# Optimization experiments

Hardware: AMD Instinct MI355X
Metric: run time of the kernel (lower is better)

The kernel has to match this reference:

```python
import jax, jax.numpy as jnp
import numpy as np

E = 384      # embed_dim
H = 8        # num_heads
D = E // H   # head_dim = 48
G = 16       # grid_size
HT = 128     # height
WD = 128     # width
FF = 1536
B = 8
EPS = 1e-5


def _ln(x, g, b):
    m = jnp.mean(x, axis=-1, keepdims=True)
    v = jnp.mean(jnp.square(x - m), axis=-1, keepdims=True)
    return (x - m) * jax.lax.rsqrt(v + EPS) * g + b


def _grid_attention(xn, in_proj_w, in_proj_b, out_w, out_b):
    # xn: [B, S, E] with S = HT*WD. Extract 16x16 windows -> [Wn, B, T, E]
    nh, nw = HT // G, WD // G
    T = G * G
    xw = xn.reshape(B, nh, G, nw, G, E).transpose(1, 3, 0, 2, 4, 5)
    xw = xw.reshape(nh * nw, B, T, E)  # [Wn, B, T, E]
    # torch in_proj: qkv = x @ W.T + b, W: [3E, E]
    qkv = jnp.einsum('wbte,fe->wbtf', xw, in_proj_w) + in_proj_b
    q, k, v = jnp.split(qkv, 3, axis=-1)
    q = q.reshape(nh * nw, B, T, H, D)
    k = k.reshape(nh * nw, B, T, H, D)
    v = v.reshape(nh * nw, B, T, H, D)
    scale = 1.0 / jnp.sqrt(jnp.asarray(D, dtype=xn.dtype))
    # NOTE: torch MHA (batch_first=False) treats dim0 of (B, T, E) as seq len,
    # so attention mixes across the batch axis (length B) per window position.
    scores = jnp.einsum('wbtnd,wctnd->wtnbc', q, k) * scale  # [Wn,T,H,B,B]
    p = jax.nn.softmax(scores, axis=-1)
    o = jnp.einsum('wtnbc,wctnd->wbtnd', p, v).reshape(nh * nw, B, T, E)
    o = jnp.einsum('wbte,fe->wbtf', o, out_w) + out_b
    # reassemble windows back to [B, S, E]
    o = o.reshape(nh, nw, B, G, G, E).transpose(2, 0, 3, 1, 4, 5)
    return o.reshape(B, HT * WD, E)


def setup_inputs() -> dict:
    key = jax.random.key(0)
    ks = jax.random.split(key, 6)
    S = HT * WD
    return {
        'x': jax.random.normal(ks[0], (B, S, E), jnp.float32),
        'in_proj_w': jax.random.normal(ks[1], (3 * E, E), jnp.float32) * 0.02,
        'in_proj_b': jnp.zeros((3 * E,), jnp.float32),
        'out_w': jax.random.normal(ks[2], (E, E), jnp.float32) * 0.02,
        'out_b': jnp.zeros((E,), jnp.float32),
        'ln1_g': jnp.ones((E,), jnp.float32),
        'ln1_b': jnp.zeros((E,), jnp.float32),
        'ln2_g': jnp.ones((E,), jnp.float32),
        'ln2_b': jnp.zeros((E,), jnp.float32),
        'w1': jax.random.normal(ks[3], (FF, E), jnp.float32) * 0.02,
        'b1': jnp.zeros((FF,), jnp.float32),
        'w2': jax.random.normal(ks[4], (E, FF), jnp.float32) * 0.02,
        'b2': jnp.zeros((E,), jnp.float32),
    }


def reference(x, in_proj_w, in_proj_b, out_w, out_b, ln1_g, ln1_b,
              ln2_g, ln2_b, w1, b1, w2, b2):
    # Pre-attn LN, windowed MHA (eval mode: dropout off), residual
    attn = _grid_attention(_ln(x, ln1_g, ln1_b), in_proj_w, in_proj_b, out_w, out_b)
    x = x + attn
    # LN + GELU MLP (exact erf gelu, torch nn.GELU default) + residual
    h = _ln(x, ln2_g, ln2_b)
    h = jax.nn.gelu(jnp.einsum('bse,fe->bsf', h, w1) + b1, approximate=False)
    h = jnp.einsum('bsf,ef->bse', h, w2) + b2
    return x + h
```

## Files before the change

kernel.cpp:

```cpp
#include <hip/hip_runtime.h>
#include <hip/hip_bf16.h>
#include <math.h>

typedef unsigned short u16;
typedef __attribute__((ext_vector_type(8))) short short8;
typedef __attribute__((ext_vector_type(4))) float floatx4;

__device__ __forceinline__ float bf2f(u16 u) {
  union { unsigned int i; float f; } w; w.i = ((unsigned int)u) << 16; return w.f;
}
__device__ __forceinline__ u16 f2bf(float f) {
  union { float f; unsigned int i; } w; w.f = f;
  unsigned int r = (w.i + 0x7fffu + ((w.i >> 16) & 1u)) >> 16;
  return (u16)r;
}

__global__ void detect_k(const unsigned int* __restrict__ xw, int* __restrict__ flag) {
  __shared__ int cnt;
  if (threadIdx.x == 0) cnt = 0;
  __syncthreads();
  int c = 0;
  for (int i = threadIdx.x; i < 4096; i += 256) {
    const unsigned int e = (xw[i] >> 7) & 0xffu;
    c += (e >= 0x71u && e <= 0x81u) ? 1 : 0;
  }
  atomicAdd(&cnt, c);
  __syncthreads();
  if (threadIdx.x == 0) flag[0] = (cnt > 2048) ? 1 : 0;
}

__global__ void conv_k(const void* __restrict__ src, u16* __restrict__ dst, int n,
                       const int* __restrict__ flagp) {
  const int dt = flagp[0];
  const int stride = gridDim.x * blockDim.x;
  for (int i = blockIdx.x * blockDim.x + threadIdx.x; i < n; i += stride)
    dst[i] = dt ? ((const u16*)src)[i] : f2bf(((const float*)src)[i]);
}

#define BM 256
#define BN 128
#define BK 32

#define CSW(r) (((r) & 3) ^ ((((r) >> 2) & 1) << 1))

template<int MODE>
__global__ __launch_bounds__(512, 4) void gemm_bt(
    const u16* __restrict__ A, const u16* __restrict__ Bt,
    const u16* __restrict__ bias, const void* res,
    void* C, int M, int N, int K, int s0, int lsc, int jump,
    const int* __restrict__ flagp)
{
  __shared__ __align__(16) u16 lA[2][BM * BK];
  __shared__ __align__(16) u16 lB[2][BN * BK];
  const int tid  = threadIdx.x;
  const int lane = tid & 63;
  const int w    = tid >> 6;
  const int wm   = (w >> 1) * 64;
  const int wn   = (w & 1) * 64;

  const int nbn = N / BN;
  const int nwg = gridDim.x;
  const int q = nwg >> 3, r = nwg & 7;
  const int xcd = blockIdx.x & 7, lid = blockIdx.x >> 3;
  const int gid = (xcd < r ? xcd * (q + 1) : r * (q + 1) + (xcd - r) * q) + lid;
  const long mbase = (long)(gid / nbn) * BM;
  const long nbase = (long)(gid % nbn) * BN;
  const int dt = (MODE == 1) ? flagp[0] : 0;

  floatx4 acc[4][4] = {};

  const int rl  = lane >> 2;
  const int sl  = lane & 3;
  const int frm = lane & 15;
  const int fkg = lane >> 4;

  const int nk = K / BK;

  auto STAGE = [&](int buf, int k0) {
    #pragma unroll
    for (int j = 0; j < 2; ++j) {
      const int R   = w * 32 + j * 16;
      const int row = R + rl;
      const int kg  = sl ^ CSW(row);
      const u16* gp = A + (mbase + row) * (long)K + (k0 + kg * 8);
      __builtin_amdgcn_global_load_lds(
          (const __attribute__((address_space(1))) void*)gp,
          (__attribute__((address_space(3))) void*)(&lA[buf][R * BK]),
          16, 0, 0);
    }
    {
      const int R   = w * 16;
      const int row = R + rl;
      const int kg  = sl ^ CSW(row);
      const u16* gp = Bt + (nbase + row) * (long)K + (k0 + kg * 8);
      __builtin_amdgcn_global_load_lds(
          (const __attribute__((address_space(1))) void*)gp,
          (__attribute__((address_space(3))) void*)(&lB[buf][R * BK]),
          16, 0, 0);
    }
  };

  auto COMPUTE = [&](int buf) {
    short8 af[4], bfr[4];
    #pragma unroll
    for (int i = 0; i < 4; ++i) {
      const int rm = wm + i * 16 + frm;
      af[i] = *(const short8*)(&lA[buf][rm * BK + ((fkg ^ CSW(rm)) * 8)]);
      const int rn = wn + i * 16 + frm;
      bfr[i] = *(const short8*)(&lB[buf][rn * BK + ((fkg ^ CSW(rn)) * 8)]);
    }
    #pragma unroll
    for (int i = 0; i < 4; ++i)
      #pragma unroll
      for (int n = 0; n < 4; ++n)
        acc[i][n] = __builtin_amdgcn_mfma_f32_16x16x32_bf16(
            af[i], bfr[n], acc[i][n], 0, 0, 0);
  };

  STAGE(0, 0);
  __syncthreads();
  int cur = 0;
  for (int t = 0; t < nk - 1; ++t) {
    STAGE(cur ^ 1, (t + 1) * BK);
    COMPUTE(cur);
    __syncthreads();
    cur ^= 1;
  }
  COMPUTE(cur);

  float bv[4];
  #pragma unroll
  for (int n = 0; n < 4; ++n)
    bv[n] = bf2f(bias[nbase + wn + n * 16 + frm]);

  #pragma unroll
  for (int i = 0; i < 4; ++i) {
    #pragma unroll
    for (int n = 0; n < 4; ++n) {
      const long col = nbase + wn + n * 16 + frm;
      #pragma unroll
      for (int r4 = 0; r4 < 4; ++r4) {
        const long row = mbase + wm + i * 16 + (lane >> 4) * 4 + r4;
        float v = acc[i][n][r4] + bv[n];
        if (MODE == 2) v = 0.5f * v * (1.f + erff(v * 0.70710678118654752f));
        if (MODE == 1) {
          const long g   = row + s0 + ((row >> lsc) * (long)jump);
          const long idx = g * (long)N + col;
          if (dt) { v += bf2f(((const u16*)res)[idx]); ((u16*)C)[idx] = f2bf(v); }
          else    { v += ((const float*)res)[idx];     ((float*)C)[idx] = v;     }
        } else {
          ((u16*)C)[row * (long)N + col] = f2bf(v);
        }
      }
    }
  }
}

__global__ __launch_bounds__(256) void ln_k(
    const void* __restrict__ xin, const u16* __restrict__ g,
    const u16* __restrict__ b, u16* __restrict__ y,
    int s0, int lsc, int jump, const int* __restrict__ flagp)
{
  const int dt   = flagp[0];
  const int lane = threadIdx.x & 63;
  const int wv   = threadIdx.x >> 6;
  const long r   = (long)blockIdx.x * 4 + wv;
  const long gr  = r + s0 + ((r >> lsc) * (long)jump);
  float v[6];
  float s = 0.f;
  if (dt) {
    const u16* xp = (const u16*)xin + gr * 384;
    #pragma unroll
    for (int j = 0; j < 3; ++j) {
      const unsigned int u = *(const unsigned int*)(xp + lane * 2 + 128 * j);
      v[2 * j]     = bf2f((u16)(u & 0xffffu));
      v[2 * j + 1] = bf2f((u16)(u >> 16));
      s += v[2 * j] + v[2 * j + 1];
    }
  } else {
    const float* xf = (const float*)xin + gr * 384;
    #pragma unroll
    for (int j = 0; j < 3; ++j) {
      const float2 ld = *(const float2*)(xf + lane * 2 + 128 * j);
      v[2 * j] = ld.x; v[2 * j + 1] = ld.y;
      s += ld.x + ld.y;
    }
  }
  #pragma unroll
  for (int o = 32; o; o >>= 1) s += __shfl_xor(s, o, 64);
  const float mean = s * (1.f / 384.f);
  float vs = 0.f;
  #pragma unroll
  for (int j = 0; j < 6; ++j) { const float d = v[j] - mean; vs += d * d; }
  #pragma unroll
  for (int o = 32; o; o >>= 1) vs += __shfl_xor(vs, o, 64);
  const float rstd = rsqrtf(vs * (1.f / 384.f) + 1e-5f);
  u16* yp = y + r * 384;
  #pragma unroll
  for (int j = 0; j < 3; ++j) {
    const int e = lane * 2 + 128 * j;
    const float o0 = (v[2 * j]     - mean) * rstd * bf2f(g[e])     + bf2f(b[e]);
    const float o1 = (v[2 * j + 1] - mean) * rstd * bf2f(g[e + 1]) + bf2f(b[e + 1]);
    *(unsigned int*)(yp + e) = (unsigned int)f2bf(o0) | ((unsigned int)f2bf(o1) << 16);
  }
}

__global__ __launch_bounds__(512) void attn_k(
    const u16* __restrict__ qkv, u16* __restrict__ o, int sc)
{
  __shared__ __align__(16) u16 sm[8 * 1160];
  const int tid = threadIdx.x;
  const int sl = blockIdx.x;
  for (int u = tid; u < 1152; u += 512) {
    const int b   = u / 144;
    const int c16 = u - b * 144;
    const int4 val = *(const int4*)(qkv + ((size_t)(b * sc + sl)) * 1152 + c16 * 8);
    *(int4*)(sm + b * 1160 + c16 * 8) = val;
  }
  __syncthreads();
  const int lane = tid & 63;
  const int h = tid >> 6;
  const int b = lane >> 3;
  const int c = lane & 7;
  const u16* qrow = sm + b * 1160 + h * 48;
  const u16* krow = sm + c * 1160 + 384 + h * 48;
  float scv = 0.f;
  #pragma unroll
  for (int dd = 0; dd < 6; ++dd) {
    const short8 q8 = *(const short8*)(qrow + dd * 8);
    const short8 k8 = *(const short8*)(krow + dd * 8);
    #pragma unroll
    for (int e = 0; e < 8; ++e)
      scv += bf2f((u16)q8[e]) * bf2f((u16)k8[e]);
  }
  scv *= 0.14433756729740643f;
  float mx = scv;
  mx = fmaxf(mx, __shfl_xor(mx, 1, 64));
  mx = fmaxf(mx, __shfl_xor(mx, 2, 64));
  mx = fmaxf(mx, __shfl_xor(mx, 4, 64));
  const float ex = expf(scv - mx);
  float sum = ex;
  sum += __shfl_xor(sum, 1, 64);
  sum += __shfl_xor(sum, 2, 64);
  sum += __shfl_xor(sum, 4, 64);
  const float p = ex / sum;
  float pc[8];
  #pragma unroll
  for (int cc = 0; cc < 8; ++cc) pc[cc] = __shfl(p, (b << 3) | cc, 64);
  if (c < 6) {
    const int dg = c;
    float oacc[8] = {0, 0, 0, 0, 0, 0, 0, 0};
    #pragma unroll
    for (int cc = 0; cc < 8; ++cc) {
      const short8 v8 = *(const short8*)(sm + cc * 1160 + 768 + h * 48 + dg * 8);
      #pragma unroll
      for (int e = 0; e < 8; ++e) oacc[e] += pc[cc] * bf2f((u16)v8[e]);
    }
    short8 rv;
    #pragma unroll
    for (int e = 0; e < 8; ++e) rv[e] = (short)f2bf(oacc[e]);
    *(short8*)(o + ((size_t)(b * sc + sl)) * 384 + h * 48 + dg * 8) = rv;
  }
}

extern "C" void kernel_launch(void* const* d_in, const int* in_sizes, int n_in,
                              void* d_out, int out_size, void* d_ws, size_t ws_size,
                              hipStream_t stream) {
  (void)in_sizes; (void)n_in; (void)out_size;
  int* flag = (int*)d_ws;
  u16* W    = (u16*)d_ws + 16;
  static const int woff[12] = {0, 442368, 443520, 590976, 591360, 591744,
                               592128, 592512, 592896, 1182720, 1184256, 1774080};
  static const int wlen[12] = {442368, 1152, 147456, 384, 384, 384,
                               384, 384, 589824, 1536, 589824, 384};
  u16* SCR = W + 1774464;
  const size_t used = (size_t)((char*)SCR - (char*)d_ws);
  const size_t avail = (ws_size > used) ? (ws_size - used) : 0;

  detect_k<<<1, 256, 0, stream>>>((const unsigned int*)d_in[0], flag);
  for (int i = 0; i < 12; ++i) {
    const int n  = wlen[i];
    const int nb = (n + 1023) / 1024;
    conv_k<<<(nb < 512 ? nb : 512), 256, 0, stream>>>(d_in[i + 1], W + woff[i], n, flag);
  }
  const u16 *ipw = W + woff[0], *ipb = W + woff[1], *outw = W + woff[2],
            *outb = W + woff[3], *l1g = W + woff[4], *l1b = W + woff[5],
            *l2g = W + woff[6], *l2b = W + woff[7], *w1 = W + woff[8],
            *b1 = W + woff[9], *w2 = W + woff[10], *b2 = W + woff[11];
  const void* x = d_in[0];

  int sc = 16384;
  while (sc > 32 && (size_t)24576 * (size_t)sc > avail) sc >>= 1;
  const int lsc  = 31 - __builtin_clz((unsigned)sc);
  const int jump = 16384 - sc;
  u16* QKV = SCR;
  u16* XO  = QKV + (size_t)9216 * sc;

  for (int c = 0; c < 16384 / sc; ++c) {
    const int s0 = c * sc;
    const int Mc = 8 * sc;
    ln_k<<<Mc / 4, 256, 0, stream>>>(x, l1g, l1b, XO, s0, lsc, jump, flag);
    gemm_bt<0><<<(Mc / 256) * 9, 512, 0, stream>>>(
        XO, ipw, ipb, nullptr, QKV, Mc, 1152, 384, 0, 0, 0, flag);
    attn_k<<<sc, 512, 0, stream>>>(QKV, XO, sc);
    gemm_bt<1><<<(Mc / 256) * 3, 512, 0, stream>>>(
        XO, outw, outb, x, d_out, Mc, 384, 384, s0, lsc, jump, flag);
  }

  long Mt = (long)(avail / 3840);
  if (Mt > 131072) Mt = 131072;
  if (Mt < 256)    Mt = 256;
  while (Mt & (Mt - 1)) Mt &= Mt - 1;
  u16* Hb = SCR;
  u16* H1 = Hb + (size_t)Mt * 384;

  for (long t0 = 0; t0 < 131072; t0 += Mt) {
    const int Mtc = (int)((131072 - t0 < Mt) ? (131072 - t0) : Mt);
    ln_k<<<Mtc / 4, 256, 0, stream>>>(d_out, l2g, l2b, Hb, (int)t0, 30, 0, flag);
    gemm_bt<2><<<(Mtc / 256) * 12, 512, 0, stream>>>(
        Hb, w1, b1, nullptr, H1, Mtc, 1536, 384, 0, 0, 0, flag);
    gemm_bt<1><<<(Mtc / 256) * 3, 512, 0, stream>>>(
        H1, w2, b2, d_out, d_out, Mtc, 384, 1536, (int)t0, 30, 0, flag);
  }
}
```

Measured before the change: 1.658 ms.

## Load A fragments directly from global and stage large B chunks in LDS

```diff
diff --git a/kernel.cpp b/kernel.cpp
--- a/kernel.cpp
+++ b/kernel.cpp
@@ -39,9 +39,7 @@
 
 #define BM 256
 #define BN 128
-#define BK 32
-
-#define CSW(r) (((r) & 3) ^ ((((r) >> 2) & 1) << 1))
+#define KC 192
 
 template<int MODE>
 __global__ __launch_bounds__(512, 4) void gemm_bt(
@@ -50,8 +48,7 @@
     void* C, int M, int N, int K, int s0, int lsc, int jump,
     const int* __restrict__ flagp)
 {
-  __shared__ __align__(16) u16 lA[2][BM * BK];
-  __shared__ __align__(16) u16 lB[2][BN * BK];
+  __shared__ __align__(16) u16 lB[BN * KC];
   const int tid  = threadIdx.x;
   const int lane = tid & 63;
   const int w    = tid >> 6;
@@ -69,64 +66,55 @@
 
   floatx4 acc[4][4] = {};
 
-  const int rl  = lane >> 2;
-  const int sl  = lane & 3;
   const int frm = lane & 15;
   const int fkg = lane >> 4;
 
-  const int nk = K / BK;
-
-  auto STAGE = [&](int buf, int k0) {
-    #pragma unroll
-    for (int j = 0; j < 2; ++j) {
-      const int R   = w * 32 + j * 16;
-      const int row = R + rl;
-      const int kg  = sl ^ CSW(row);
-      const u16* gp = A + (mbase + row) * (long)K + (k0 + kg * 8);
-      __builtin_amdgcn_global_load_lds(
-          (const __attribute__((address_space(1))) void*)gp,
-          (__attribute__((address_space(3))) void*)(&lA[buf][R * BK]),
-          16, 0, 0);
-    }
+  const u16* pA0 = A + (mbase + wm +  0 + frm) * (long)K + fkg * 8;
+  const u16* pA1 = A + (mbase + wm + 16 + frm) * (long)K + fkg * 8;
+  const u16* pA2 = A + (mbase + wm + 32 + frm) * (long)K + fkg * 8;
+  const u16* pA3 = A + (mbase + wm + 48 + frm) * (long)K + fkg * 8;
+
+  const int nchunk = K / KC;
+
+  for (int kc = 0; kc < nchunk; ++kc) {
+    if (kc > 0) __syncthreads();
     {
-      const int R   = w * 16;
-      const int row = R + rl;
-      const int kg  = sl ^ CSW(row);
-      const u16* gp = Bt + (nbase + row) * (long)K + (k0 + kg * 8);
-      __builtin_amdgcn_global_load_lds(
-          (const __attribute__((address_space(1))) void*)gp,
-          (__attribute__((address_space(3))) void*)(&lB[buf][R * BK]),
-          16, 0, 0);
-    }
-  };
-
-  auto COMPUTE = [&](int buf) {
-    short8 af[4], bfr[4];
-    #pragma unroll
-    for (int i = 0; i < 4; ++i) {
-      const int rm = wm + i * 16 + frm;
-      af[i] = *(const short8*)(&lA[buf][rm * BK + ((fkg ^ CSW(rm)) * 8)]);
-      const int rn = wn + i * 16 + frm;
-      bfr[i] = *(const short8*)(&lB[buf][rn * BK + ((fkg ^ CSW(rn)) * 8)]);
-    }
-    #pragma unroll
-    for (int i = 0; i < 4; ++i)
+      const long kcoff = (long)kc * KC;
       #pragma unroll
-      for (int n = 0; n < 4; ++n)
-        acc[i][n] = __builtin_amdgcn_mfma_f32_16x16x32_bf16(
-            af[i], bfr[n], acc[i][n], 0, 0, 0);
-  };
-
-  STAGE(0, 0);
-  __syncthreads();
-  int cur = 0;
-  for (int t = 0; t < nk - 1; ++t) {
-    STAGE(cur ^ 1, (t + 1) * BK);
-    COMPUTE(cur);
+      for (int j = 0; j < 6; ++j) {
+        const int unit = w * 384 + j * 64 + lane;
+        const int rloc = unit / 24;
+        const int s    = unit - rloc * 24;
+        const int kg   = (s & ~7) | ((s & 7) ^ (rloc & 7));
+        const u16* gp  = Bt + (nbase + rloc) * (long)K + kcoff + kg * 8;
+        __builtin_amdgcn_global_load_lds(
+            (const __attribute__((address_space(1))) void*)gp,
+            (__attribute__((address_space(3))) void*)(&lB[(w * 384 + j * 64) * 8]),
+            16, 0, 0);
+      }
+    }
     __syncthreads();
-    cur ^= 1;
-  }
-  COMPUTE(cur);
+
+    #pragma unroll
+    for (int t = 0; t < 6; ++t) {
+      short8 a0 = *(const short8*)(pA0 + t * 32);
+      short8 a1 = *(const short8*)(pA1 + t * 32);
+      short8 a2 = *(const short8*)(pA2 + t * 32);
+      short8 a3 = *(const short8*)(pA3 + t * 32);
+      #pragma unroll
+      for (int n = 0; n < 4; ++n) {
+        const int rn = wn + n * 16 + frm;
+        const int ks = t * 4 + fkg;
+        const int sw = (ks & ~7) | ((ks & 7) ^ (rn & 7));
+        const short8 bfr = *(const short8*)(&lB[rn * KC + sw * 8]);
+        acc[0][n] = __builtin_amdgcn_mfma_f32_16x16x32_bf16(a0, bfr, acc[0][n], 0, 0, 0);
+        acc[1][n] = __builtin_amdgcn_mfma_f32_16x16x32_bf16(a1, bfr, acc[1][n], 0, 0, 0);
+        acc[2][n] = __builtin_amdgcn_mfma_f32_16x16x32_bf16(a2, bfr, acc[2][n], 0, 0, 0);
+        acc[3][n] = __builtin_amdgcn_mfma_f32_16x16x32_bf16(a3, bfr, acc[3][n], 0, 0, 0);
+      }
+    }
+    pA0 += KC; pA1 += KC; pA2 += KC; pA3 += KC;
+  }
 
   float bv[4];
   #pragma unroll
```

Result: slower. 2.488 ms (+50.1%).
